# Performance work log

Hardware: AMD Instinct MI355X
Metric: run time of the kernel (lower is better)

Reference implementation:

```python
import jax, jax.numpy as jnp
import numpy as np

N = 50000


def gcn_conv(x, edge_index, W, b):
    # x: [N, F_in], edge_index: [2, E] (row=source j, col=target i)
    n = x.shape[0]
    loops = jnp.arange(n, dtype=edge_index.dtype)
    row = jnp.concatenate([edge_index[0], loops])
    col = jnp.concatenate([edge_index[1], loops])
    # linear transform first (PyG GCNConv)
    xw = x @ W  # [N, F_out]
    # symmetric normalization deg^{-1/2}[row] * deg^{-1/2}[col]
    deg = jax.ops.segment_sum(jnp.ones_like(col, dtype=xw.dtype), col, num_segments=n)
    dis = jnp.where(deg > 0, jax.lax.rsqrt(jnp.maximum(deg, 1e-12)), 0.0)
    norm = dis[row] * dis[col]  # [E+N]
    # gather-scale-scatter: sum_j norm_ij * (W x_j)
    msgs = xw[row] * norm[:, None]
    out = jax.ops.segment_sum(msgs, col, num_segments=n)
    return out + b


def setup_inputs() -> dict:
    key = jax.random.key(0)
    k1, k2, k3, k4, k5 = jax.random.split(key, 5)
    in_dim, hidden_dim, out_dim = 128, 128, 64
    x = jax.random.normal(k1, (N, in_dim), dtype=jnp.float32)
    edge_index = jax.random.randint(k2, (2, 800000), 0, N, dtype=jnp.int64)
    s1 = 1.0 / np.sqrt(in_dim)
    s2 = 1.0 / np.sqrt(hidden_dim)
    W1 = jax.random.uniform(k3, (in_dim, hidden_dim), jnp.float32, -s1, s1)
    b1 = jnp.zeros((hidden_dim,), jnp.float32)
    W2 = jax.random.uniform(k4, (hidden_dim, out_dim), jnp.float32, -s2, s2)
    b2 = jnp.zeros((out_dim,), jnp.float32)
    return {"x": x, "edge_index": edge_index, "W1": W1, "b1": b1, "W2": W2, "b2": b2}


def reference(x, edge_index, W1, b1, W2, b2):
    h = gcn_conv(x, edge_index, W1, b1)
    h = jax.nn.relu(h)
    # dropout(p=0.5, training=False) -> identity (inference reference)
    out = gcn_conv(h, edge_index, W2, b2)
    return out
```

## Files before the change

### kernel.cpp

```cpp
#include <hip/hip_runtime.h>
#include <hip/hip_fp16.h>


typedef _Float16 half8 __attribute__((ext_vector_type(8)));
typedef float floatx4 __attribute__((ext_vector_type(4)));

__global__ void k_count(const int* __restrict__ col, int* __restrict__ deg,
                        int* __restrict__ rank, int E) {
    int e = blockIdx.x * blockDim.x + threadIdx.x;
    if (e < E) rank[e] = atomicAdd(&deg[col[e]], 1);
}

__global__ void k_dis(const int* __restrict__ deg, float* __restrict__ dis, int n) {
    int i = blockIdx.x * blockDim.x + threadIdx.x;
    if (i < n) dis[i] = rsqrtf((float)deg[i] + 1.0f);
}

__global__ __launch_bounds__(1024) void k_scan_local(const int* __restrict__ deg,
                                                     int* __restrict__ rowptr,
                                                     int* __restrict__ bsum, int n) {
    __shared__ int s[1024];
    int b = blockIdx.x, tid = threadIdx.x;
    int i = b * 1024 + tid;
    int v = (i < n) ? deg[i] : 0;
    s[tid] = v;
    __syncthreads();
    for (int off = 1; off < 1024; off <<= 1) {
        int t = (tid >= off) ? s[tid - off] : 0;
        __syncthreads();
        s[tid] += t;
        __syncthreads();
    }
    if (i < n) rowptr[i + 1] = s[tid];
    if (tid == 1023) bsum[b] = s[1023];
    if (b == 0 && tid == 0) rowptr[0] = 0;
}

__global__ __launch_bounds__(256) void k_scan_fix(int* __restrict__ rowptr,
                                                  const int* __restrict__ bsum, int n) {
    __shared__ int red[256];
    int b = blockIdx.x, tid = threadIdx.x;
    int partial = 0;
    for (int j = tid; j < b; j += 256) partial += bsum[j];
    red[tid] = partial;
    __syncthreads();
    for (int off = 128; off > 0; off >>= 1) {
        if (tid < off) red[tid] += red[tid + off];
        __syncthreads();
    }
    int offv = red[0];
    if (offv == 0) return;
#pragma unroll
    for (int r = 0; r < 4; ++r) {
        int i = b * 1024 + r * 256 + tid;
        if (i < n) rowptr[i + 1] += offv;
    }
}

__global__ void k_fill(const int* __restrict__ row, const int* __restrict__ col,
                       const int* __restrict__ rowptr, const int* __restrict__ rank,
                       int* __restrict__ csr, int E) {
    int e = blockIdx.x * blockDim.x + threadIdx.x;
    if (e < E) csr[rowptr[col[e]] + rank[e]] = row[e];
}

template <int N, typename AT>
__global__ __launch_bounds__(256) void k_gemm_mfma(const AT* __restrict__ X,
                                                   const float* __restrict__ W,
                                                   const float* __restrict__ scale,
                                                   __half* __restrict__ Y, int M) {
    __shared__ __align__(16) __half2 wt[N * 64];
    int tid = threadIdx.x;
    for (int i = tid; i < N * 64; i += 256) {
        int n = i & (N - 1);
        int k2 = i / N;
        float w0 = W[(size_t)(2 * k2) * N + n];
        float w1 = W[(size_t)(2 * k2 + 1) * N + n];
        wt[n * 64 + ((k2 >> 2) ^ (n & 15)) * 4 + (k2 & 3)] = __floats2half2_rn(w0, w1);
    }
    __syncthreads();

    int wid = tid >> 6, lane = tid & 63;
    int col = lane & 15, quad = lane >> 4;
    int m_a = blockIdx.x * 64 + wid * 16 + col;
    bool a_ok = m_a < M;
    constexpr int NT = N / 16;
    floatx4 acc[NT] = {};
#pragma unroll
    for (int ks = 0; ks < 4; ++ks) {
        int k = ks * 32 + quad * 8;
        half8 af;
        if constexpr (sizeof(AT) == 4) {
            floatx4 a0 = {0.f, 0.f, 0.f, 0.f}, a1 = {0.f, 0.f, 0.f, 0.f};
            if (a_ok) {
                a0 = *(const floatx4*)&X[(size_t)m_a * 128 + k];
                a1 = *(const floatx4*)&X[(size_t)m_a * 128 + k + 4];
            }
            af = half8{(_Float16)a0[0], (_Float16)a0[1], (_Float16)a0[2], (_Float16)a0[3],
                       (_Float16)a1[0], (_Float16)a1[1], (_Float16)a1[2], (_Float16)a1[3]};
        } else {
            half8 t = {};
            if (a_ok) t = *(const half8*)(const void*)&X[(size_t)m_a * 128 + k];
            af = t;
        }
        int kblk = ks * 4 + quad;
#pragma unroll
        for (int nt = 0; nt < NT; ++nt) {
            int n = nt * 16 + col;
            half8 bf = *(const half8*)(const void*)&wt[n * 64 + (kblk ^ (n & 15)) * 4];
            acc[nt] = __builtin_amdgcn_mfma_f32_16x16x32_f16(af, bf, acc[nt], 0, 0, 0);
        }
    }
    int mbase = blockIdx.x * 64 + wid * 16 + quad * 4;
    float s[4];
#pragma unroll
    for (int r = 0; r < 4; ++r) s[r] = (mbase + r < M) ? scale[mbase + r] : 0.f;
#pragma unroll
    for (int nt = 0; nt < NT; ++nt) {
#pragma unroll
        for (int r = 0; r < 4; ++r) {
            if (mbase + r < M)
                Y[(size_t)(mbase + r) * N + nt * 16 + col] = __float2half(acc[nt][r] * s[r]);
        }
    }
}

__global__ __launch_bounds__(256) void k_agg128(const __half* __restrict__ xw,
                                                const float* __restrict__ dis,
                                                const int* __restrict__ rowptr,
                                                const int* __restrict__ csr,
                                                const float* __restrict__ bias,
                                                __half* __restrict__ out, int n) {
    int wid = (blockIdx.x << 2) | (threadIdx.x >> 6);
    int lane = threadIdx.x & 63;
    if (wid >= n) return;
    float di = dis[wid];
    int beg = rowptr[wid], end = rowptr[wid + 1];
    const __half2* xh = (const __half2*)xw;
    float2 sf = __half22float2(xh[(size_t)wid * 64 + lane]);
    float ax = sf.x, ay = sf.y;
    int e = beg;
    for (; e + 16 <= end; e += 16) {
        int s[16];
        float2 v[16];
#pragma unroll
        for (int j = 0; j < 16; ++j) s[j] = csr[e + j];
#pragma unroll
        for (int j = 0; j < 16; ++j) v[j] = __half22float2(xh[(size_t)s[j] * 64 + lane]);
#pragma unroll
        for (int j = 0; j < 16; ++j) { ax += v[j].x; ay += v[j].y; }
    }
    for (; e + 4 <= end; e += 4) {
        int s[4];
        float2 v[4];
#pragma unroll
        for (int j = 0; j < 4; ++j) s[j] = csr[e + j];
#pragma unroll
        for (int j = 0; j < 4; ++j) v[j] = __half22float2(xh[(size_t)s[j] * 64 + lane]);
#pragma unroll
        for (int j = 0; j < 4; ++j) { ax += v[j].x; ay += v[j].y; }
    }
    for (; e < end; ++e) {
        float2 f = __half22float2(xh[(size_t)csr[e] * 64 + lane]);
        ax += f.x;
        ay += f.y;
    }
    float2 bb = ((const float2*)bias)[lane];
    ax = fmaxf(ax * di + bb.x, 0.f);
    ay = fmaxf(ay * di + bb.y, 0.f);
    ((__half2*)out)[(size_t)wid * 64 + lane] = __floats2half2_rn(ax, ay);
}

__global__ __launch_bounds__(256) void k_agg64(const __half* __restrict__ xw,
                                               const float* __restrict__ dis,
                                               const int* __restrict__ rowptr,
                                               const int* __restrict__ csr,
                                               const float* __restrict__ bias,
                                               float* __restrict__ out, int n) {
    int tid = threadIdx.x;
    int lane = tid & 63, hl = lane & 31;
    int node = blockIdx.x * 8 + ((tid >> 6) << 1) + (lane >> 5);
    float di = 0.f;
    int beg = 0, end = 0;
    if (node < n) {
        di = dis[node];
        beg = rowptr[node];
        end = rowptr[node + 1];
    }
    int deg = end - beg;
    int mx = max(deg, __shfl(deg, lane ^ 32));
    const __half2* xh = (const __half2*)xw;
    float2 a = make_float2(0.f, 0.f);
    if (node < n) a = __half22float2(xh[(size_t)node * 32 + hl]);
    int i = 0;
    for (; i + 8 <= mx; i += 8) {
        int s[8];
        float2 v[8];
#pragma unroll
        for (int j = 0; j < 8; ++j) {
            int e = beg + i + j;
            s[j] = (e < end) ? csr[e] : 0;
        }
#pragma unroll
        for (int j = 0; j < 8; ++j) v[j] = __half22float2(xh[(size_t)s[j] * 32 + hl]);
#pragma unroll
        for (int j = 0; j < 8; ++j) {
            if (beg + i + j < end) { a.x += v[j].x; a.y += v[j].y; }
        }
    }
    for (; i < mx; ++i) {
        int e = beg + i;
        int s = (e < end) ? csr[e] : 0;
        float2 v = __half22float2(xh[(size_t)s * 32 + hl]);
        if (e < end) { a.x += v.x; a.y += v.y; }
    }
    if (node < n) {
        float2 bb = ((const float2*)bias)[hl];
        ((float2*)out)[(size_t)node * 32 + hl] =
            make_float2(a.x * di + bb.x, a.y * di + bb.y);
    }
}

extern "C" void kernel_launch(void* const* d_in, const int* in_sizes, int n_in,
                              void* d_out, int out_size, void* d_ws, size_t ws_size,
                              hipStream_t stream) {
    const float* x  = (const float*)d_in[0];
    const int*   ei = (const int*)d_in[1];
    const float* W1 = (const float*)d_in[2];
    const float* b1 = (const float*)d_in[3];
    const float* W2 = (const float*)d_in[4];
    const float* b2 = (const float*)d_in[5];
    float* out = (float*)d_out;

    const int n = in_sizes[0] / 128;
    const int E = in_sizes[1] / 2;
    const int* row = ei;
    const int* col = ei + E;
    const int NB = (n + 1023) / 1024;

    char* ws = (char*)d_ws;
    size_t off = 0;
    auto alloc = [&](size_t bytes) -> void* {
        void* p = ws + off;
        off += (bytes + 255) & ~(size_t)255;
        return p;
    };
    int*    deg    = (int*)alloc((size_t)n * 4);
    int*    rowptr = (int*)alloc((size_t)(n + 1) * 4);
    int*    bsum   = (int*)alloc((size_t)NB * 4);
    int*    rank   = (int*)alloc((size_t)E * 4);
    int*    csr    = (int*)alloc((size_t)E * 4);
    float*  dis    = (float*)alloc((size_t)n * 4);
    __half* xw1    = (__half*)alloc((size_t)n * 128 * 2);
    __half* h      = (__half*)alloc((size_t)n * 128 * 2);
    __half* xw2    = (__half*)alloc((size_t)n * 64 * 2);
    (void)ws_size;

    hipMemsetAsync(deg, 0, (size_t)n * 4, stream);
    k_count<<<(E + 255) / 256, 256, 0, stream>>>(col, deg, rank, E);
    k_dis<<<(n + 255) / 256, 256, 0, stream>>>(deg, dis, n);
    k_scan_local<<<NB, 1024, 0, stream>>>(deg, rowptr, bsum, n);
    k_scan_fix<<<NB, 256, 0, stream>>>(rowptr, bsum, n);
    k_fill<<<(E + 255) / 256, 256, 0, stream>>>(row, col, rowptr, rank, csr, E);

    int gb = (n + 63) / 64;
    k_gemm_mfma<128, float><<<gb, 256, 0, stream>>>(x, W1, dis, xw1, n);
    k_agg128<<<(n + 3) / 4, 256, 0, stream>>>(xw1, dis, rowptr, csr, b1, h, n);

    k_gemm_mfma<64, __half><<<gb, 256, 0, stream>>>(h, W2, dis, xw2, n);
    k_agg64<<<(n + 7) / 8, 256, 0, stream>>>(xw2, dis, rowptr, csr, b2, out, n);
}
```

Measured before the change: 233.3 us.

## Widen aggregation gathers to 16-byte half8 loads and fuse dis into scan

After: 215.9 us. 1.08x faster.

```diff
diff --git a/kernel.cpp b/kernel.cpp
--- a/kernel.cpp
+++ b/kernel.cpp
@@ -11,18 +11,15 @@
     if (e < E) rank[e] = atomicAdd(&deg[col[e]], 1);
 }
 
-__global__ void k_dis(const int* __restrict__ deg, float* __restrict__ dis, int n) {
-    int i = blockIdx.x * blockDim.x + threadIdx.x;
-    if (i < n) dis[i] = rsqrtf((float)deg[i] + 1.0f);
-}
-
 __global__ __launch_bounds__(1024) void k_scan_local(const int* __restrict__ deg,
                                                      int* __restrict__ rowptr,
-                                                     int* __restrict__ bsum, int n) {
+                                                     int* __restrict__ bsum,
+                                                     float* __restrict__ dis, int n) {
     __shared__ int s[1024];
     int b = blockIdx.x, tid = threadIdx.x;
     int i = b * 1024 + tid;
     int v = (i < n) ? deg[i] : 0;
+    if (i < n) dis[i] = rsqrtf((float)v + 1.0f);
     s[tid] = v;
     __syncthreads();
     for (int off = 1; off < 1024; off <<= 1) {
@@ -131,44 +128,66 @@
                                                 const int* __restrict__ csr,
                                                 const float* __restrict__ bias,
                                                 __half* __restrict__ out, int n) {
-    int wid = (blockIdx.x << 2) | (threadIdx.x >> 6);
-    int lane = threadIdx.x & 63;
-    if (wid >= n) return;
-    float di = dis[wid];
-    int beg = rowptr[wid], end = rowptr[wid + 1];
-    const __half2* xh = (const __half2*)xw;
-    float2 sf = __half22float2(xh[(size_t)wid * 64 + lane]);
-    float ax = sf.x, ay = sf.y;
-    int e = beg;
-    for (; e + 16 <= end; e += 16) {
-        int s[16];
-        float2 v[16];
-#pragma unroll
-        for (int j = 0; j < 16; ++j) s[j] = csr[e + j];
-#pragma unroll
-        for (int j = 0; j < 16; ++j) v[j] = __half22float2(xh[(size_t)s[j] * 64 + lane]);
-#pragma unroll
-        for (int j = 0; j < 16; ++j) { ax += v[j].x; ay += v[j].y; }
-    }
-    for (; e + 4 <= end; e += 4) {
-        int s[4];
-        float2 v[4];
-#pragma unroll
-        for (int j = 0; j < 4; ++j) s[j] = csr[e + j];
-#pragma unroll
-        for (int j = 0; j < 4; ++j) v[j] = __half22float2(xh[(size_t)s[j] * 64 + lane]);
-#pragma unroll
-        for (int j = 0; j < 4; ++j) { ax += v[j].x; ay += v[j].y; }
-    }
-    for (; e < end; ++e) {
-        float2 f = __half22float2(xh[(size_t)csr[e] * 64 + lane]);
-        ax += f.x;
-        ay += f.y;
-    }
-    float2 bb = ((const float2*)bias)[lane];
-    ax = fmaxf(ax * di + bb.x, 0.f);
-    ay = fmaxf(ay * di + bb.y, 0.f);
-    ((__half2*)out)[(size_t)wid * 64 + lane] = __floats2half2_rn(ax, ay);
+    int tid = threadIdx.x;
+    int lane = tid & 63;
+    int q = lane >> 4, li = lane & 15;
+    int node = blockIdx.x * 16 + ((tid >> 6) << 2) + q;
+    bool ok = node < n;
+    float di = 0.f;
+    int beg = 0, end = 0;
+    if (ok) {
+        di = dis[node];
+        beg = rowptr[node];
+        end = rowptr[node + 1];
+    }
+    int deg = end - beg;
+    int m1 = max(deg, __shfl(deg, lane ^ 16));
+    int mx = max(m1, __shfl(m1, lane ^ 32));
+    const half8* rows = (const half8*)xw;
+    float acc[8] = {};
+    if (ok) {
+        half8 sf = rows[(size_t)node * 16 + li];
+#pragma unroll
+        for (int f = 0; f < 8; ++f) acc[f] = (float)sf[f];
+    }
+    int i = 0;
+    for (; i + 8 <= mx; i += 8) {
+        int s[8];
+        half8 v[8];
+#pragma unroll
+        for (int j = 0; j < 8; ++j) {
+            int e = beg + i + j;
+            s[j] = (e < end) ? csr[e] : 0;
+        }
+#pragma unroll
+        for (int j = 0; j < 8; ++j) v[j] = rows[(size_t)s[j] * 16 + li];
+#pragma unroll
+        for (int j = 0; j < 8; ++j) {
+            if (beg + i + j < end) {
+#pragma unroll
+                for (int f = 0; f < 8; ++f) acc[f] += (float)v[j][f];
+            }
+        }
+    }
+    for (; i < mx; ++i) {
+        int e = beg + i;
+        int s = (e < end) ? csr[e] : 0;
+        half8 v = rows[(size_t)s * 16 + li];
+        if (e < end) {
+#pragma unroll
+            for (int f = 0; f < 8; ++f) acc[f] += (float)v[f];
+        }
+    }
+    if (ok) {
+        floatx4 b0 = *(const floatx4*)&bias[li * 8];
+        floatx4 b1 = *(const floatx4*)&bias[li * 8 + 4];
+        half8 o;
+#pragma unroll
+        for (int f = 0; f < 4; ++f) o[f] = (_Float16)fmaxf(acc[f] * di + b0[f], 0.f);
+#pragma unroll
+        for (int f = 0; f < 4; ++f) o[4 + f] = (_Float16)fmaxf(acc[4 + f] * di + b1[f], 0.f);
+        ((half8*)out)[(size_t)node * 16 + li] = o;
+    }
 }
 
 __global__ __launch_bounds__(256) void k_agg64(const __half* __restrict__ xw,
@@ -178,46 +197,66 @@
                                                const float* __restrict__ bias,
                                                float* __restrict__ out, int n) {
     int tid = threadIdx.x;
-    int lane = tid & 63, hl = lane & 31;
-    int node = blockIdx.x * 8 + ((tid >> 6) << 1) + (lane >> 5);
+    int lane = tid & 63;
+    int o8 = lane >> 3, li = lane & 7;
+    int node = blockIdx.x * 32 + ((tid >> 6) << 3) + o8;
+    bool ok = node < n;
     float di = 0.f;
     int beg = 0, end = 0;
-    if (node < n) {
+    if (ok) {
         di = dis[node];
         beg = rowptr[node];
         end = rowptr[node + 1];
     }
     int deg = end - beg;
-    int mx = max(deg, __shfl(deg, lane ^ 32));
-    const __half2* xh = (const __half2*)xw;
-    float2 a = make_float2(0.f, 0.f);
-    if (node < n) a = __half22float2(xh[(size_t)node * 32 + hl]);
+    int m1 = max(deg, __shfl(deg, lane ^ 8));
+    int m2 = max(m1, __shfl(m1, lane ^ 16));
+    int mx = max(m2, __shfl(m2, lane ^ 32));
+    const half8* rows = (const half8*)xw;
+    float acc[8] = {};
+    if (ok) {
+        half8 sf = rows[(size_t)node * 8 + li];
+#pragma unroll
+        for (int f = 0; f < 8; ++f) acc[f] = (float)sf[f];
+    }
     int i = 0;
     for (; i + 8 <= mx; i += 8) {
         int s[8];
-        float2 v[8];
+        half8 v[8];
 #pragma unroll
         for (int j = 0; j < 8; ++j) {
             int e = beg + i + j;
             s[j] = (e < end) ? csr[e] : 0;
         }
 #pragma unroll
-        for (int j = 0; j < 8; ++j) v[j] = __half22float2(xh[(size_t)s[j] * 32 + hl]);
+        for (int j = 0; j < 8; ++j) v[j] = rows[(size_t)s[j] * 8 + li];
 #pragma unroll
         for (int j = 0; j < 8; ++j) {
-            if (beg + i + j < end) { a.x += v[j].x; a.y += v[j].y; }
+            if (beg + i + j < end) {
+#pragma unroll
+                for (int f = 0; f < 8; ++f) acc[f] += (float)v[j][f];
+            }
         }
     }
     for (; i < mx; ++i) {
         int e = beg + i;
         int s = (e < end) ? csr[e] : 0;
-        float2 v = __half22float2(xh[(size_t)s * 32 + hl]);
-        if (e < end) { a.x += v.x; a.y += v.y; }
-    }
-    if (node < n) {
-        float2 bb = ((const float2*)bias)[hl];
-        ((float2*)out)[(size_t)node * 32 + hl] =
-            make_float2(a.x * di + bb.x, a.y * di + bb.y);
+        half8 v = rows[(size_t)s * 8 + li];
+        if (e < end) {
+#pragma unroll
+            for (int f = 0; f < 8; ++f) acc[f] += (float)v[f];
+        }
+    }
+    if (ok) {
+        floatx4 b0 = *(const floatx4*)&bias[li * 8];
+        floatx4 b1 = *(const floatx4*)&bias[li * 8 + 4];
+        floatx4 o0, o1;
+#pragma unroll
+        for (int f = 0; f < 4; ++f) o0[f] = acc[f] * di + b0[f];
+#pragma unroll
+        for (int f = 0; f < 4; ++f) o1[f] = acc[4 + f] * di + b1[f];
+        *(floatx4*)&out[(size_t)node * 64 + li * 8] = o0;
+        *(floatx4*)&out[(size_t)node * 64 + li * 8 + 4] = o1;
     }
 }
 
@@ -258,15 +297,14 @@
 
     hipMemsetAsync(deg, 0, (size_t)n * 4, stream);
     k_count<<<(E + 255) / 256, 256, 0, stream>>>(col, deg, rank, E);
-    k_dis<<<(n + 255) / 256, 256, 0, stream>>>(deg, dis, n);
-    k_scan_local<<<NB, 1024, 0, stream>>>(deg, rowptr, bsum, n);
+    k_scan_local<<<NB, 1024, 0, stream>>>(deg, rowptr, bsum, dis, n);
     k_scan_fix<<<NB, 256, 0, stream>>>(rowptr, bsum, n);
     k_fill<<<(E + 255) / 256, 256, 0, stream>>>(row, col, rowptr, rank, csr, E);
 
     int gb = (n + 63) / 64;
     k_gemm_mfma<128, float><<<gb, 256, 0, stream>>>(x, W1, dis, xw1, n);
-    k_agg128<<<(n + 3) / 4, 256, 0, stream>>>(xw1, dis, rowptr, csr, b1, h, n);
+    k_agg128<<<(n + 15) / 16, 256, 0, stream>>>(xw1, dis, rowptr, csr, b1, h, n);
 
     k_gemm_mfma<64, __half><<<gb, 256, 0, stream>>>(h, W2, dis, xw2, n);
-    k_agg64<<<(n + 7) / 8, 256, 0, stream>>>(xw2, dis, rowptr, csr, b2, out, n);
-}
+    k_agg64<<<(n + 31) / 32, 256, 0, stream>>>(xw2, dis, rowptr, csr, b2, out, n);
+}
```
